# Kernel tuning notes

Measured on AMD Instinct MI355X. Metric: run time of the kernel, lower is better.

The kernel has to match this reference:

```python
import jax, jax.numpy as jnp
import numpy as np

D, H, N, T, B = 32, 128, 128, 256, 64   # input_dim, n_units, N_units, time_depth, batch
HEADS, THR, SHORT = 4, 0.01, 2
HD = H // HEADS


def setup_inputs() -> dict:
    key = jax.random.key(0)
    ks = iter(jax.random.split(key, 64))
    rn = lambda *s: jax.random.normal(next(ks), s, dtype=jnp.float32) * 0.1
    inp = {"x": jax.random.normal(next(ks), (B, T, D), dtype=jnp.float32)}
    for n_ in ["U_j", "U_i", "U_f", "U_o"]:
        inp[n_] = rn(D, 1, H)
    for n_ in ["W_j", "W_i", "W_f", "W_o"]:
        inp[n_] = rn(D, H, H)
    for n_ in ["B_j", "B_i", "B_f", "B_o"]:
        inp[n_] = jnp.full((D, H), 0.01, dtype=jnp.float32)
    for n_ in ["u_j", "u_i", "u_f", "u_o"]:
        inp[n_] = rn(D, N)
    for n_ in ["w_j", "w_i", "w_f", "w_o"]:
        inp[n_] = rn(N, N)
    for n_ in ["b_j", "b_i", "b_f", "b_o"]:
        inp[n_] = jnp.full((N,), 0.01, dtype=jnp.float32)
    inp["qkv_w"] = rn(3 * H, H)      # nn.Linear(H, 3H, bias=False) weight
    inp["out_w"] = rn(H, H)          # attn out_proj weight
    inp["h_proj_w"] = rn(N, H)       # nn.Linear(H, N, bias=False) weight
    inp["w_p"] = rn(N, 1)
    inp["b_p"] = jnp.zeros((1,), dtype=jnp.float32)
    return inp


def reference(x, U_j, U_i, U_f, U_o, W_j, W_i, W_f, W_o, B_j, B_i, B_f, B_o,
              u_j, u_i, u_f, u_o, w_j, w_i, w_f, w_o, b_j, b_i, b_f, b_o,
              qkv_w, out_w, h_proj_w, w_p, b_p):
    scale = 1.0 / jnp.sqrt(jnp.asarray(HD, dtype=x.dtype))

    def attention(h):  # h: (B, D, H) -> (B, D, H) cross-variable MHA
        qkv = h @ qkv_w.T                              # (B, D, 3H)
        q, k, v = jnp.split(qkv, 3, axis=-1)
        rs = lambda a: a.reshape(h.shape[0], D, HEADS, HD).transpose(0, 2, 1, 3)
        q, k, v = rs(q), rs(k), rs(v)                  # (B, heads, D, HD)
        scores = jnp.einsum('bhid,bhjd->bhij', q, k) * scale
        a = jax.nn.softmax(scores, axis=-1)
        a = jnp.where(a >= THR, a, jnp.zeros_like(a))
        ctx = jnp.einsum('bhij,bhjd->bhid', a, v)      # (B, heads, D, HD)
        ctx = ctx.transpose(0, 2, 1, 3).reshape(h.shape[0], D, H)
        return ctx @ out_w.T

    # per-variable input contributions: x_t[:, :, None] * U[:, 0, :]
    Uj, Ui, Uf, Uo = U_j[:, 0, :], U_i[:, 0, :], U_f[:, 0, :], U_o[:, 0, :]

    def step(carry, inputs):
        t, x_t = inputs                                # x_t: (B, D)
        h_var, c_var, h_mix, c_mix = carry
        xu = x_t[:, :, None]                            # (B, D, 1)
        j_var = jnp.tanh(jnp.einsum('bij,ijk->bik', h_var, W_j) + xu * Uj + B_j)
        i_var = jax.nn.sigmoid(jnp.einsum('bij,ijk->bik', h_var, W_i) + xu * Ui + B_i)
        f_var = jax.nn.sigmoid(jnp.einsum('bij,ijk->bik', h_var, W_f) + xu * Uf + B_f)
        o_var = jax.nn.sigmoid(jnp.einsum('bij,ijk->bik', h_var, W_o) + xu * Uo + B_o)
        c_var = c_var * f_var + i_var * j_var
        h_var = o_var * jnp.tanh(c_var)

        i_t = jax.nn.sigmoid(x_t @ u_i + h_mix @ w_i + b_i)
        f_t = jax.nn.sigmoid(x_t @ u_f + h_mix @ w_f + b_f)
        o_t = jax.nn.sigmoid(x_t @ u_o + h_mix @ w_o + b_o)
        j_t = jnp.tanh(x_t @ u_j + h_mix @ w_j + b_j)
        c_mix = f_t * c_mix + i_t * j_t
        h_mix_lstm = o_t * jnp.tanh(c_mix)

        z = attention(h_var)
        h_hat = z.mean(axis=1) @ h_proj_w.T            # (B, N)
        pred = h_hat @ w_p + b_p                       # (B, 1)
        h_mix = jnp.where(t > SHORT, h_hat, h_mix_lstm)
        return (h_var, c_var, h_mix, c_mix), pred

    z32 = jnp.zeros((x.shape[0], D, H), dtype=x.dtype)
    carry0 = (z32, z32,
              jnp.zeros((x.shape[0], N), dtype=x.dtype),
              jnp.zeros((x.shape[0], N), dtype=x.dtype))
    ts = jnp.arange(T - 1)
    xs = x.transpose(1, 0, 2)[: T - 1]                 # (T-1, B, D)
    _, preds = jax.lax.scan(step, carry0, (ts, xs))    # (T-1, B, 1)
    pred = preds[SHORT + 1:].transpose(1, 0, 2)        # (B, T-SHORT-2, 1)
    return pred
```

## Files before the change

kernel.cpp:

```cpp
#include <hip/hip_runtime.h>
#include <hip/hip_bf16.h>

typedef __hip_bfloat16 bf16;
typedef _Float16 f16x2 __attribute__((ext_vector_type(2)));
typedef _Float16 half8 __attribute__((ext_vector_type(8)));
typedef float f32x4 __attribute__((ext_vector_type(4)));

#define D_ 32
#define H_ 128
#define T_ 256
#define B_ 64
#define NSTEP 255
#define NOUT 252

#define F32_PROBE 0x3C23D70Au

#define MFMA_F16(A, B, C) __builtin_amdgcn_mfma_f32_16x16x32_f16(A, B, C, 0, 0, 0)

__device__ __forceinline__ float sigm(float v) {
    return __builtin_amdgcn_rcpf(1.0f + __expf(-v));
}
__device__ __forceinline__ float tanh_f(float x) {
    float xc = fminf(fmaxf(x, -9.0f), 9.0f);
    float e = __expf(-2.0f * xc);
    return (1.0f - e) * __builtin_amdgcn_rcpf(1.0f + e);
}

__device__ __forceinline__ unsigned int packh2(float a, float b) {
    union { unsigned int u; f16x2 h; } c;
    c.h[0] = (_Float16)a; c.h[1] = (_Float16)b;
    return c.u;
}
union U4H8 { uint4 u; half8 h; };
__device__ __forceinline__ half8 as_h8(uint4 u) { U4H8 x; x.u = u; return x.h; }

struct CvtArgs {
    const void* src[18];
    float* dst[18];
    int cnt[18];
    const unsigned int* probe;
};

__global__ __launch_bounds__(256) void k_convert(CvtArgs a)
{
    const bool isf32 = (*a.probe == F32_PROBE);
    const int seg = blockIdx.y;
    const int n = a.cnt[seg];
    const void* s = a.src[seg];
    float* dgt = a.dst[seg];
    for (int i = blockIdx.x * 256 + threadIdx.x; i < n; i += gridDim.x * 256) {
        float v;
        if (isf32) v = ((const float*)s)[i];
        else       v = __uint_as_float(((unsigned int)((const unsigned short*)s)[i]) << 16);
        dgt[i] = v;
    }
}

__global__ __launch_bounds__(256) void k_xpose(const float* __restrict__ xf,
                                              float* __restrict__ xT)
{
    __shared__ float tile[64][33];
    const int t = blockIdx.x;
    const int tid = threadIdx.x;
    for (int idx = tid; idx < 2048; idx += 256) {
        int b = idx >> 5, dd = idx & 31;
        tile[b][dd] = xf[((size_t)b * T_ + t) * D_ + dd];
    }
    __syncthreads();
    for (int idx = tid; idx < 2048; idx += 256) {
        int dd = idx >> 6, b = idx & 63;
        xT[((size_t)dd * T_ + t) * B_ + b] = tile[b][dd];
    }
}

__global__ __launch_bounds__(256) void k_pack(const float* __restrict__ qw,
                                              unsigned int* __restrict__ wpk)
{
    int idx = blockIdx.x * 256 + threadIdx.x;
    int e   = idx & 3;
    int w4  = idx >> 2;
    int l15 = w4 & 15;
    int l4  = (w4 >> 4) & 3;
    int ks  = (w4 >> 6) & 3;
    int mt  = w4 >> 8;
    int r   = mt * 16 + l15;
    int k2  = (ks * 4 + l4) * 4 + e;
    wpk[idx] = packh2(qw[r * 128 + 2 * k2], qw[r * 128 + 2 * k2 + 1]);
}

__global__ __launch_bounds__(1024, 1) void k_recur(
    const float* __restrict__ xT, const float* __restrict__ wf,
    const float* __restrict__ uf, const float* __restrict__ bfv,
    float* __restrict__ cstg, unsigned int* __restrict__ h2g,
    unsigned int* __restrict__ hbw,
    int t0, int t1, int slots)
{
    __shared__ __align__(16) unsigned int hsw[2][512];
    __shared__ float xs[2048];

    const int tid  = threadIdx.x;
    const int lane = tid & 63;
    const int w    = tid >> 6;
    const int bx   = blockIdx.x;
    const int d    = bx >> 3;
    const int b0   = (bx & 7) * 8;
    const int l15  = lane & 15;
    const int l4   = lane >> 4;
    const int bb   = l15 & 7;
    const int sel  = l15 >> 3;

    const int ntot = (t1 - t0) * 8;
    for (int idx = tid; idx < ntot; idx += 1024) {
        int tr = idx >> 3, bbx = idx & 7;
        xs[idx] = xT[((size_t)d * T_ + (t0 + tr)) * B_ + b0 + bbx];
    }

    uint4 wfr[2][4];
    #pragma unroll
    for (int mtl = 0; mtl < 2; ++mtl) {
        const int c = w * 32 + mtl * 16 + l15;
        const int g = c & 3, h = c >> 2;
        const float* Wp = wf + (((size_t)g * 32 + d) * 128) * 128 + h;
        #pragma unroll
        for (int ks = 0; ks < 4; ++ks) {
            const int jb = ks * 32 + l4 * 8;
            uint4 u;
            u.x = packh2(Wp[(jb + 0) * 128], Wp[(jb + 1) * 128]);
            u.y = packh2(Wp[(jb + 2) * 128], Wp[(jb + 3) * 128]);
            u.z = packh2(Wp[(jb + 4) * 128], Wp[(jb + 5) * 128]);
            u.w = packh2(Wp[(jb + 6) * 128], Wp[(jb + 7) * 128]);
            wfr[mtl][ks] = u;
        }
    }
    float ur[2][4], br[2][4];
    #pragma unroll
    for (int mtl = 0; mtl < 2; ++mtl) {
        const int hq = w * 8 + mtl * 4 + l4;
        #pragma unroll
        for (int g = 0; g < 4; ++g) {
            ur[mtl][g] = uf [g * 4096 + d * H_ + hq];
            br[mtl][g] = bfv[g * 4096 + d * H_ + hq];
        }
    }

    float cs0;
    if (t0 == 0) cs0 = 0.f;
    else         cs0 = cstg[bx * 1024 + tid];

    {
        unsigned int* tgt = hsw[t0 & 1];
        if (t0 == 0) { if (tid < 512) tgt[tid] = 0u; }
        else         { if (tid < 512) tgt[tid] = h2g[bx * 512 + tid]; }
    }
    __syncthreads();

    const int wrd = sel * 2 + (l4 >> 1);
    const bool writer = !(l4 & 1);
    unsigned int pend = 0u;

    for (int t = t0; t < t1; ++t) {
        if (t > t0 && writer) {
            const int tp = t - 1;
            if (tp >= 3) {
                const int slotp = (tp - 3) % slots;
                hbw[((((size_t)slotp * B_ + b0 + bb) * 16 + w) * 32 + d) * 4 + wrd] = pend;
            }
        }

        const unsigned int* hr = hsw[t & 1];
        unsigned int* hw       = hsw[(t & 1) ^ 1];

        uint4 hb[4];
        #pragma unroll
        for (int ks = 0; ks < 4; ++ks) {
            const int jc = ks * 4 + l4;
            hb[ks] = *(const uint4*)&hr[bb * 64 + (((jc ^ bb) & 15) << 2)];
        }
        const float xb = xs[(t - t0) * 8 + bb];

        f32x4 acc[2];
        #pragma unroll
        for (int mtl = 0; mtl < 2; ++mtl) {
            f32x4 a;
            a[0] = xb * ur[mtl][0] + br[mtl][0];
            a[1] = xb * ur[mtl][1] + br[mtl][1];
            a[2] = xb * ur[mtl][2] + br[mtl][2];
            a[3] = xb * ur[mtl][3] + br[mtl][3];
            acc[mtl] = a;
        }
        #pragma unroll
        for (int ks = 0; ks < 4; ++ks) {
            #pragma unroll
            for (int mtl = 0; mtl < 2; ++mtl)
                acc[mtl] = MFMA_F16(as_h8(wfr[mtl][ks]), as_h8(hb[ks]), acc[mtl]);
        }

        float a0 = sel ? acc[1][0] : acc[0][0];
        float a1 = sel ? acc[1][1] : acc[0][1];
        float a2 = sel ? acc[1][2] : acc[0][2];
        float a3 = sel ? acc[1][3] : acc[0][3];
        float jj = tanh_f(a0);
        float ii = sigm(a1);
        float ff = sigm(a2);
        float oo = sigm(a3);
        float cn = cs0 * ff + ii * jj;
        cs0 = cn;
        float hv = oo * tanh_f(cn);
        float pv = __shfl_xor(hv, 16);
        if (writer) {
            unsigned int hp = packh2(hv, pv);
            hw[bb * 64 + (((w ^ bb) & 15) << 2) + wrd] = hp;
            pend = hp;
        }
        __syncthreads();
    }

    {
        const int tp = t1 - 1;
        if (tp >= 3 && writer) {
            const int slotp = (tp - 3) % slots;
            hbw[((((size_t)slotp * B_ + b0 + bb) * 16 + w) * 32 + d) * 4 + wrd] = pend;
        }
    }

    {
        const unsigned int* fin = hsw[t1 & 1];
        if (tid < 512) h2g[bx * 512 + tid] = fin[tid];
        cstg[bx * 1024 + tid] = cs0;
    }
}

#define QK_OFF  0
#define VT_OFF  16384
#define A_OFF   0
#define RED_OFF 24576
#define ATT_LDS 24640
#define TT_     4

__global__ __launch_bounds__(256, 2) void k_attn(
    const unsigned int* __restrict__ hbuf, const unsigned int* __restrict__ wpk,
    const float* __restrict__ vc, const unsigned int* __restrict__ probe,
    void* __restrict__ outv, int t0, int slots, int nt)
{
    __shared__ __align__(16) char S[ATT_LDS];

    const int tid  = threadIdx.x;
    const int lane = tid & 63;
    const int w    = tid >> 6;
    const int b    = blockIdx.y;
    const int tbase = t0 + TT_ * blockIdx.x;
    int ntt = nt - TT_ * (int)blockIdx.x;
    if (ntt > TT_) ntt = TT_;
    const int l15  = lane & 15;
    const int l4   = lane >> 4;

    uint4 wfr[6][4];
    #pragma unroll
    for (int mi = 0; mi < 6; ++mi) {
        #pragma unroll
        for (int ks = 0; ks < 4; ++ks)
            wfr[mi][ks] = ((const uint4*)wpk)[((w + 4 * mi) * 4 + ks) * 64 + lane];
    }
    const float vcr0 = vc[w * 32 + l15];
    const float vcr1 = vc[w * 32 + 16 + l15];

    for (int tt = 0; tt < ntt; ++tt) {
        if (tt) __syncthreads();

        const int t = tbase + tt;
        const int slot = (t - 3) % slots;
        const uint4* hsrc4 =
            (const uint4*)hbuf + ((size_t)slot * B_ + b) * 512;
        uint4 hfr[2][4];
        #pragma unroll
        for (int nt_ = 0; nt_ < 2; ++nt_) {
            #pragma unroll
            for (int ks = 0; ks < 4; ++ks)
                hfr[nt_][ks] = hsrc4[(ks * 4 + l4) * 32 + nt_ * 16 + l15];
        }
        #pragma unroll
        for (int mi = 0; mi < 6; ++mi) {
            const int mt  = w + 4 * mi;
            const int r0  = mt * 16 + (l4 << 2);
            const int tau = r0 >> 7;
            const int hd2 = (r0 >> 5) & 3;
            const int d0  = r0 & 31;
            #pragma unroll
            for (int nt_ = 0; nt_ < 2; ++nt_) {
                f32x4 acc = {0.f, 0.f, 0.f, 0.f};
                #pragma unroll
                for (int ks = 0; ks < 4; ++ks)
                    acc = MFMA_F16(as_h8(wfr[mi][ks]), as_h8(hfr[nt_][ks]), acc);
                const int ddc = nt_ * 16 + l15;
                if (tau < 2) {
                    unsigned int u0 = packh2(acc[0], acc[1]);
                    unsigned int u1 = packh2(acc[2], acc[3]);
                    const int c = (d0 >> 3) ^ ((ddc >> 1) & 3);
                    *(uint2*)(S + QK_OFF + (tau * 4 + hd2) * 2048 + ddc * 64
                              + c * 16 + ((2 * d0) & 15)) = make_uint2(u0, u1);
                } else {
                    #pragma unroll
                    for (int q = 0; q < 4; ++q) {
                        const int j = d0 + q;
                        const int c = (ddc >> 3) ^ ((j >> 1) & 3);
                        *(_Float16*)(S + VT_OFF + hd2 * 2048 + j * 64
                                     + c * 16 + ((2 * ddc) & 15)) = (_Float16)acc[q];
                    }
                }
            }
        }
        __syncthreads();

        uint4 qa[2], ka[2];
        #pragma unroll
        for (int It = 0; It < 2; ++It) {
            const int dd = It * 16 + l15;
            const int c = l4 ^ ((dd >> 1) & 3);
            qa[It] = *(const uint4*)(S + QK_OFF + (0 * 4 + w) * 2048 + dd * 64 + c * 16);
            ka[It] = *(const uint4*)(S + QK_OFF + (1 * 4 + w) * 2048 + dd * 64 + c * 16);
        }
        f32x4 st[2][2];
        #pragma unroll
        for (int Et = 0; Et < 2; ++Et)
            #pragma unroll
            for (int It = 0; It < 2; ++It) {
                f32x4 z = {0.f, 0.f, 0.f, 0.f};
                st[Et][It] = MFMA_F16(as_h8(ka[Et]), as_h8(qa[It]), z);
            }
        const float scale = 0.17677669529663687f;
        float mx[2], sum[2];
        #pragma unroll
        for (int It = 0; It < 2; ++It) {
            float m = -1e30f;
            #pragma unroll
            for (int Et = 0; Et < 2; ++Et)
                #pragma unroll
                for (int q = 0; q < 4; ++q) {
                    st[Et][It][q] *= scale;
                    m = fmaxf(m, st[Et][It][q]);
                }
            m = fmaxf(m, __shfl_xor(m, 16));
            m = fmaxf(m, __shfl_xor(m, 32));
            mx[It] = m;
        }
        #pragma unroll
        for (int It = 0; It < 2; ++It) {
            float s = 0.f;
            #pragma unroll
            for (int Et = 0; Et < 2; ++Et)
                #pragma unroll
                for (int q = 0; q < 4; ++q) {
                    float e = __expf(st[Et][It][q] - mx[It]);
                    st[Et][It][q] = e;
                    s += e;
                }
            s += __shfl_xor(s, 16);
            s += __shfl_xor(s, 32);
            sum[It] = s;
        }
        const float inv0 = 1.0f / sum[0];
        const float inv1 = 1.0f / sum[1];
        #pragma unroll
        for (int It = 0; It < 2; ++It) {
            const int i = It * 16 + l15;
            const float inv = It ? inv1 : inv0;
            #pragma unroll
            for (int Et = 0; Et < 2; ++Et)
                #pragma unroll
                for (int q = 0; q < 4; ++q) {
                    float a = st[Et][It][q] * inv;
                    if (a < 0.01f) a = 0.f;
                    const int e = Et * 16 + (l4 << 2) + q;
                    const int c = (e >> 3) ^ ((i >> 1) & 3);
                    *(_Float16*)(S + A_OFF + w * 2048 + i * 64
                                 + c * 16 + ((2 * e) & 15)) = (_Float16)a;
                }
        }
        uint4 aa[2], vb[2];
        #pragma unroll
        for (int It = 0; It < 2; ++It) {
            const int i = It * 16 + l15;
            const int c = l4 ^ ((i >> 1) & 3);
            aa[It] = *(const uint4*)(S + A_OFF + w * 2048 + i * 64 + c * 16);
        }
        #pragma unroll
        for (int Jt = 0; Jt < 2; ++Jt) {
            const int j = Jt * 16 + l15;
            const int c = l4 ^ ((j >> 1) & 3);
            vb[Jt] = *(const uint4*)(S + VT_OFF + w * 2048 + j * 64 + c * 16);
        }
        f32x4 ct[2][2];
        #pragma unroll
        for (int It = 0; It < 2; ++It)
            #pragma unroll
            for (int Jt = 0; Jt < 2; ++Jt) {
                f32x4 z = {0.f, 0.f, 0.f, 0.f};
                ct[It][Jt] = MFMA_F16(as_h8(aa[It]), as_h8(vb[Jt]), z);
            }
        float p = 0.f;
        #pragma unroll
        for (int Jt = 0; Jt < 2; ++Jt) {
            float cs_ = 0.f;
            #pragma unroll
            for (int It = 0; It < 2; ++It)
                #pragma unroll
                for (int q = 0; q < 4; ++q) cs_ += ct[It][Jt][q];
            cs_ += __shfl_xor(cs_, 16);
            cs_ += __shfl_xor(cs_, 32);
            p += cs_ * (Jt ? vcr1 : vcr0);
        }
        p *= (1.0f / 32.0f);
        p += __shfl_xor(p, 1);
        p += __shfl_xor(p, 2);
        p += __shfl_xor(p, 4);
        p += __shfl_xor(p, 8);
        if (lane == 0)
            *(float*)(S + RED_OFF + (tt * 4 + w) * 4) = p;
    }
    __syncthreads();

    if (tid < ntt) {
        const float* rd = (const float*)(S + RED_OFF);
        float r = rd[tid * 4] + rd[tid * 4 + 1] + rd[tid * 4 + 2] + rd[tid * 4 + 3]
                + vc[128];
        const int t = tbase + tid;
        size_t oidx = (size_t)b * NOUT + (t - 3);
        if (*probe == F32_PROBE) ((float*)outv)[oidx] = r;
        else                     ((bf16*)outv)[oidx]  = __float2bfloat16(r);
    }
}

__global__ __launch_bounds__(128) void k_vcomb(
    const float* __restrict__ hprj, const float* __restrict__ outw,
    const float* __restrict__ wp, const float* __restrict__ bp,
    float* __restrict__ vc)
{
    __shared__ float tmp[128];
    int j = threadIdx.x;
    float s = 0.f;
    for (int n = 0; n < 128; ++n) s += hprj[n * 128 + j] * wp[n];
    tmp[j] = s;
    __syncthreads();
    float v = 0.f;
    for (int c = 0; c < 128; ++c) v += outw[c * 128 + j] * tmp[c];
    vc[j] = v;
    if (j == 0) vc[128] = bp[0];
}

extern "C" void kernel_launch(void* const* d_in, const int* in_sizes, int n_in,
                              void* d_out, int out_size, void* d_ws, size_t ws_size,
                              hipStream_t stream)
{
    float* ws = (float*)d_ws;
    float* xf    = ws;
    float* cstg  = ws;
    unsigned int* h2g = (unsigned int*)(ws + 262144);
    float* xT    = ws + 524288;
    float* wf    = ws + 1048576;
    float* uf    = ws + 3145728;
    float* bfv   = ws + 3162112;
    float* qkvwf = ws + 3178496;
    float* outwf = ws + 3227648;
    float* hprjf = ws + 3244032;
    float* wpf   = ws + 3260416;
    float* bpf   = ws + 3260544;
    float* vcomb = ws + 3260608;
    unsigned int* wpk = (unsigned int*)(ws + 3260800);
    unsigned short* hbuf = (unsigned short*)((char*)d_ws + 13141504);

    const unsigned int* probe = (const unsigned int*)d_in[9];

    CvtArgs ca;
    ca.src[0] = d_in[0];  ca.dst[0] = xf;  ca.cnt[0] = B_ * T_ * D_;
    for (int g = 0; g < 4; ++g) {
        ca.src[1 + g] = d_in[5 + g]; ca.dst[1 + g] = wf + (size_t)g * 524288; ca.cnt[1 + g] = 524288;
        ca.src[5 + g] = d_in[1 + g]; ca.dst[5 + g] = uf + g * 4096;           ca.cnt[5 + g] = 4096;
        ca.src[9 + g] = d_in[9 + g]; ca.dst[9 + g] = bfv + g * 4096;          ca.cnt[9 + g] = 4096;
    }
    ca.src[13] = d_in[25]; ca.dst[13] = qkvwf; ca.cnt[13] = 49152;
    ca.src[14] = d_in[26]; ca.dst[14] = outwf; ca.cnt[14] = 16384;
    ca.src[15] = d_in[27]; ca.dst[15] = hprjf; ca.cnt[15] = 16384;
    ca.src[16] = d_in[28]; ca.dst[16] = wpf;   ca.cnt[16] = 128;
    ca.src[17] = d_in[29]; ca.dst[17] = bpf;   ca.cnt[17] = 1;
    ca.probe = probe;

    k_convert<<<dim3(64, 18), dim3(256), 0, stream>>>(ca);
    k_xpose<<<dim3(T_), dim3(256), 0, stream>>>(xf, xT);
    k_pack<<<dim3(96), dim3(256), 0, stream>>>(qkvwf, wpk);
    k_vcomb<<<dim3(1), dim3(128), 0, stream>>>(hprjf, outwf, wpf, bpf, vcomb);

    long avail = (long)ws_size - 13141504L;
    int cap = (avail > 0) ? (int)(avail / 524288L) : 0;
    if (cap > NOUT) cap = NOUT;
    if (cap < 1) cap = 1;

    int t0c = 0;
    while (t0c < NSTEP) {
        int prod0 = (t0c < 3) ? 3 : t0c;
        int t1c = prod0 + cap;
        if (t1c > NSTEP) t1c = NSTEP;
        int nt = t1c - prod0;
        k_recur<<<dim3(256), dim3(1024), 0, stream>>>(
            xT, wf, uf, bfv, cstg, h2g, (unsigned int*)hbuf, t0c, t1c, cap);
        k_attn<<<dim3((nt + TT_ - 1) / TT_, 64), dim3(256), 0, stream>>>(
            (const unsigned int*)hbuf, wpk, vcomb, probe, d_out, prod0, cap, nt);
        t0c = t1c;
    }
}
```

Baseline: 449.3 us.

## Merge prep kernels, drop modulo in recur store, prefetch h in attn

The transpose, weight-pack and vcomb prep kernels are merged into one launch split by block index, removing two launch overheads. In k_recur the per-step slot modulo and index math are replaced with an incrementing pointer that wraps around. In k_attn the hidden-state fragments for the next timestep are loaded into a double buffer while the current step computes, hiding global load latency at the cost of extra registers.

```diff
diff --git a/kernel.cpp b/kernel.cpp
--- a/kernel.cpp
+++ b/kernel.cpp
@@ -56,36 +56,54 @@
     }
 }
 
-__global__ __launch_bounds__(256) void k_xpose(const float* __restrict__ xf,
-                                              float* __restrict__ xT)
+__global__ __launch_bounds__(256) void k_aux(
+    const float* __restrict__ xf, float* __restrict__ xT,
+    const float* __restrict__ qw, unsigned int* __restrict__ wpk,
+    const float* __restrict__ hprj, const float* __restrict__ outw,
+    const float* __restrict__ wp, const float* __restrict__ bp,
+    float* __restrict__ vc)
 {
     __shared__ float tile[64][33];
-    const int t = blockIdx.x;
+    const int bx = blockIdx.x;
     const int tid = threadIdx.x;
-    for (int idx = tid; idx < 2048; idx += 256) {
-        int b = idx >> 5, dd = idx & 31;
-        tile[b][dd] = xf[((size_t)b * T_ + t) * D_ + dd];
-    }
-    __syncthreads();
-    for (int idx = tid; idx < 2048; idx += 256) {
-        int dd = idx >> 6, b = idx & 63;
-        xT[((size_t)dd * T_ + t) * B_ + b] = tile[b][dd];
-    }
-}
-
-__global__ __launch_bounds__(256) void k_pack(const float* __restrict__ qw,
-                                              unsigned int* __restrict__ wpk)
-{
-    int idx = blockIdx.x * 256 + threadIdx.x;
-    int e   = idx & 3;
-    int w4  = idx >> 2;
-    int l15 = w4 & 15;
-    int l4  = (w4 >> 4) & 3;
-    int ks  = (w4 >> 6) & 3;
-    int mt  = w4 >> 8;
-    int r   = mt * 16 + l15;
-    int k2  = (ks * 4 + l4) * 4 + e;
-    wpk[idx] = packh2(qw[r * 128 + 2 * k2], qw[r * 128 + 2 * k2 + 1]);
+
+    if (bx < 256) {
+        const int t = bx;
+        for (int idx = tid; idx < 2048; idx += 256) {
+            int b = idx >> 5, dd = idx & 31;
+            tile[b][dd] = xf[((size_t)b * T_ + t) * D_ + dd];
+        }
+        __syncthreads();
+        for (int idx = tid; idx < 2048; idx += 256) {
+            int dd = idx >> 6, b = idx & 63;
+            xT[((size_t)dd * T_ + t) * B_ + b] = tile[b][dd];
+        }
+    } else if (bx < 352) {
+        int idx = (bx - 256) * 256 + tid;
+        int e   = idx & 3;
+        int w4  = idx >> 2;
+        int l15 = w4 & 15;
+        int l4  = (w4 >> 4) & 3;
+        int ks  = (w4 >> 6) & 3;
+        int mt  = w4 >> 8;
+        int r   = mt * 16 + l15;
+        int k2  = (ks * 4 + l4) * 4 + e;
+        wpk[idx] = packh2(qw[r * 128 + 2 * k2], qw[r * 128 + 2 * k2 + 1]);
+    } else {
+        float* tmp = &tile[0][0];
+        float s = 0.f;
+        if (tid < 128) {
+            for (int n = 0; n < 128; ++n) s += hprj[n * 128 + tid] * wp[n];
+            tmp[tid] = s;
+        }
+        __syncthreads();
+        if (tid < 128) {
+            float v = 0.f;
+            for (int c = 0; c < 128; ++c) v += outw[c * 128 + tid] * tmp[c];
+            vc[tid] = v;
+            if (tid == 0) vc[128] = bp[0];
+        }
+    }
 }
 
 __global__ __launch_bounds__(1024, 1) void k_recur(
@@ -158,12 +176,20 @@
     const bool writer = !(l4 & 1);
     unsigned int pend = 0u;
 
+    int sp = 0;
+    { int t0m3 = t0 - 3; if (t0m3 > 0) sp = t0m3 % slots; }
+    const size_t HSTRIDE = (size_t)B_ * 16 * 32 * 4;
+    unsigned int* const hb0 =
+        hbw + ((((size_t)b0 + bb) * 16 + w) * 32 + d) * 4 + wrd;
+    unsigned int* hbp = hb0 + (size_t)sp * HSTRIDE;
+
     for (int t = t0; t < t1; ++t) {
-        if (t > t0 && writer) {
+        if (t > t0) {
             const int tp = t - 1;
             if (tp >= 3) {
-                const int slotp = (tp - 3) % slots;
-                hbw[((((size_t)slotp * B_ + b0 + bb) * 16 + w) * 32 + d) * 4 + wrd] = pend;
+                if (writer) *hbp = pend;
+                ++sp; hbp += HSTRIDE;
+                if (sp == slots) { sp = 0; hbp = hb0; }
             }
         }
 
@@ -217,10 +243,7 @@
 
     {
         const int tp = t1 - 1;
-        if (tp >= 3 && writer) {
-            const int slotp = (tp - 3) % slots;
-            hbw[((((size_t)slotp * B_ + b0 + bb) * 16 + w) * 32 + d) * 4 + wrd] = pend;
-        }
+        if (tp >= 3 && writer) *hbp = pend;
     }
 
     {
@@ -264,20 +287,34 @@
     const float vcr0 = vc[w * 32 + l15];
     const float vcr1 = vc[w * 32 + 16 + l15];
 
-    for (int tt = 0; tt < ntt; ++tt) {
+    const int s0 = (tbase - 3) % slots;
+    const uint4* const hb4 = (const uint4*)hbuf;
+
+    uint4 hfr[2][2][4];
+    {
+        const uint4* hp = hb4 + ((size_t)s0 * B_ + b) * 512;
+        #pragma unroll
+        for (int nt_ = 0; nt_ < 2; ++nt_)
+            #pragma unroll
+            for (int ks = 0; ks < 4; ++ks)
+                hfr[0][nt_][ks] = hp[(ks * 4 + l4) * 32 + nt_ * 16 + l15];
+    }
+
+    #pragma unroll
+    for (int tt = 0; tt < TT_; ++tt) {
+        if (tt >= ntt) break;
         if (tt) __syncthreads();
 
-        const int t = tbase + tt;
-        const int slot = (t - 3) % slots;
-        const uint4* hsrc4 =
-            (const uint4*)hbuf + ((size_t)slot * B_ + b) * 512;
-        uint4 hfr[2][4];
-        #pragma unroll
-        for (int nt_ = 0; nt_ < 2; ++nt_) {
-            #pragma unroll
-            for (int ks = 0; ks < 4; ++ks)
-                hfr[nt_][ks] = hsrc4[(ks * 4 + l4) * 32 + nt_ * 16 + l15];
-        }
+        if (tt + 1 < ntt) {
+            int sn = s0 + tt + 1; if (sn >= slots) sn -= slots;
+            const uint4* hp = hb4 + ((size_t)sn * B_ + b) * 512;
+            #pragma unroll
+            for (int nt_ = 0; nt_ < 2; ++nt_)
+                #pragma unroll
+                for (int ks = 0; ks < 4; ++ks)
+                    hfr[(tt + 1) & 1][nt_][ks] = hp[(ks * 4 + l4) * 32 + nt_ * 16 + l15];
+        }
+
         #pragma unroll
         for (int mi = 0; mi < 6; ++mi) {
             const int mt  = w + 4 * mi;
@@ -290,7 +327,7 @@
                 f32x4 acc = {0.f, 0.f, 0.f, 0.f};
                 #pragma unroll
                 for (int ks = 0; ks < 4; ++ks)
-                    acc = MFMA_F16(as_h8(wfr[mi][ks]), as_h8(hfr[nt_][ks]), acc);
+                    acc = MFMA_F16(as_h8(wfr[mi][ks]), as_h8(hfr[tt & 1][nt_][ks]), acc);
                 const int ddc = nt_ * 16 + l15;
                 if (tau < 2) {
                     unsigned int u0 = packh2(acc[0], acc[1]);
@@ -428,23 +465,6 @@
         if (*probe == F32_PROBE) ((float*)outv)[oidx] = r;
         else                     ((bf16*)outv)[oidx]  = __float2bfloat16(r);
     }
-}
-
-__global__ __launch_bounds__(128) void k_vcomb(
-    const float* __restrict__ hprj, const float* __restrict__ outw,
-    const float* __restrict__ wp, const float* __restrict__ bp,
-    float* __restrict__ vc)
-{
-    __shared__ float tmp[128];
-    int j = threadIdx.x;
-    float s = 0.f;
-    for (int n = 0; n < 128; ++n) s += hprj[n * 128 + j] * wp[n];
-    tmp[j] = s;
-    __syncthreads();
-    float v = 0.f;
-    for (int c = 0; c < 128; ++c) v += outw[c * 128 + j] * tmp[c];
-    vc[j] = v;
-    if (j == 0) vc[128] = bp[0];
 }
 
 extern "C" void kernel_launch(void* const* d_in, const int* in_sizes, int n_in,
@@ -485,9 +505,8 @@
     ca.probe = probe;
 
     k_convert<<<dim3(64, 18), dim3(256), 0, stream>>>(ca);
-    k_xpose<<<dim3(T_), dim3(256), 0, stream>>>(xf, xT);
-    k_pack<<<dim3(96), dim3(256), 0, stream>>>(qkvwf, wpk);
-    k_vcomb<<<dim3(1), dim3(128), 0, stream>>>(hprjf, outwf, wpf, bpf, vcomb);
+    k_aux<<<dim3(353), dim3(256), 0, stream>>>(
+        xf, xT, qkvwf, wpk, hprjf, outwf, wpf, bpf, vcomb);
 
     long avail = (long)ws_size - 13141504L;
     int cap = (avail > 0) ? (int)(avail / 524288L) : 0;
```

Result: faster. 430.9 us (median of 2 runs) (-4.1%).
